# Kernel tuning notes

Hardware: AMD Instinct MI355X
Metric: run time of the kernel (lower is better)

Reference implementation:

```python
import jax, jax.numpy as jnp
import numpy as np


def setup_inputs() -> dict:
    key = jax.random.key(0)
    k1, k2, k3, k4 = jax.random.split(key, 4)
    B, T, C, H = 8, 2048, 1024, 128
    x = jax.random.normal(k1, (B, T, C), dtype=jnp.float32)
    Wq = jax.random.normal(k2, (C, H), dtype=jnp.float32) * (C ** -0.5)
    Wk = jax.random.normal(k3, (C, H), dtype=jnp.float32) * (C ** -0.5)
    Wv = jax.random.normal(k4, (C, H), dtype=jnp.float32) * (C ** -0.5)
    return {
        "x": x, "Wq": Wq, "Wk": Wk, "Wv": Wv,
        "gamma_fast_logit": jnp.float32(0.0),
        "gamma_medium_logit": jnp.float32(2.0),
        "gamma_slow_logit": jnp.float32(4.0),
        "alpha_logits": jnp.zeros((3,), dtype=jnp.float32),
    }


def _temporal_bias(T, gamma_fast_logit, gamma_medium_logit, gamma_slow_logit, alpha_logits):
    # delta_t[i,j] = max(i-j, 0)
    i = jnp.arange(T)[:, None]
    j = jnp.arange(T)[None, :]
    delta_t = jnp.maximum(i - j, 0).astype(jnp.float32)  # (T, T)
    gf = jax.nn.sigmoid(gamma_fast_logit) * 0.3 + 0.6
    gm = jax.nn.sigmoid(gamma_medium_logit) * 0.15 + 0.85
    gs = jax.nn.sigmoid(gamma_slow_logit) * 0.05 + 0.95
    alpha = jax.nn.softmax(alpha_logits)
    mix = (alpha[0] * jnp.power(gf, delta_t)
           + alpha[1] * jnp.power(gm, delta_t)
           + alpha[2] * jnp.power(gs, delta_t))
    return jnp.log(mix + 1e-8)  # (T, T)


def reference(x, Wq, Wk, Wv, gamma_fast_logit, gamma_medium_logit, gamma_slow_logit, alpha_logits):
    B, T, C = x.shape
    H = Wq.shape[1]
    q = x @ Wq  # (B, T, H)
    k = x @ Wk
    v = x @ Wv
    scale = H ** -0.5
    wei = jnp.einsum('bth,bsh->bts', q, k) * scale  # (B, T, T)
    bias = _temporal_bias(T, gamma_fast_logit, gamma_medium_logit, gamma_slow_logit, alpha_logits)
    wei = wei + bias[None, :, :]
    causal = jnp.tril(jnp.ones((T, T), dtype=bool))
    wei = jnp.where(causal[None, :, :], wei, -jnp.inf)
    wei = jax.nn.softmax(wei, axis=-1)
    out = jnp.einsum('bts,bsh->bth', wei, v)  # (B, T, H)
    return out
```

## Files before the change

### kernel.cpp

```cpp
#include <hip/hip_runtime.h>
#include <hip/hip_bf16.h>
#include <cstdint>

typedef __attribute__((ext_vector_type(8))) short bf16x8;
typedef __attribute__((ext_vector_type(4))) float f32x4;

#define T_SEQ 2048
#define NB    8
#define CDIM  1024
#define HDIM  128
#define NQB   32

__device__ __forceinline__ float exp2fast(float x) { return __builtin_amdgcn_exp2f(x); }
__device__ __forceinline__ float log2fast(float x) { return __builtin_amdgcn_logf(x); }

__device__ __forceinline__ short f2bf(float f) {
  unsigned u = __float_as_uint(f);
  u += 0x7fff + ((u >> 16) & 1);
  return (short)(u >> 16);
}

__device__ __forceinline__ float bf2f(short s) {
  return __uint_as_float(((unsigned)(unsigned short)s) << 16);
}

__device__ __forceinline__ unsigned pk2(float a, float b) {
  return (unsigned)(unsigned short)f2bf(a) | ((unsigned)(unsigned short)f2bf(b) << 16);
}

__device__ __forceinline__ void gload_lds16(const void* gsrc, void* lds_base_uniform) {
  __builtin_amdgcn_global_load_lds(
      (const __attribute__((address_space(1))) unsigned int*)gsrc,
      (__attribute__((address_space(3))) unsigned int*)lds_base_uniform,
      16, 0, 0);
}

__global__ void msta_bias_kernel(const float* gfl, const float* gml, const float* gsl,
                                 const float* al, float* tab) {
  int d = blockIdx.x * 256 + threadIdx.x;
  if (d >= T_SEQ) return;
  float gf = 0.30f / (1.f + __expf(-gfl[0])) + 0.60f;
  float gm = 0.15f / (1.f + __expf(-gml[0])) + 0.85f;
  float gs = 0.05f / (1.f + __expf(-gsl[0])) + 0.95f;
  float a0 = al[0], a1 = al[1], a2 = al[2];
  float mx = fmaxf(a0, fmaxf(a1, a2));
  float e0 = __expf(a0 - mx), e1 = __expf(a1 - mx), e2 = __expf(a2 - mx);
  float inv = 1.f / (e0 + e1 + e2);
  float fd = (float)d;
  float mix = e0 * inv * exp2fast(fd * log2fast(gf))
            + e1 * inv * exp2fast(fd * log2fast(gm))
            + e2 * inv * exp2fast(fd * log2fast(gs));
  tab[d] = log2fast(mix + 1e-8f);
}

__global__ void msta_wt_kernel(const float* Wq, const float* Wk, const float* Wv, short* wt) {
  int idx = blockIdx.x * 256 + threadIdx.x;
  int m = idx >> 17;
  int r = idx & 131071;
  int n = r >> 10;
  int kk = r & 1023;
  const float* W = (m == 0) ? Wq : ((m == 1) ? Wk : Wv);
  float v = W[kk * HDIM + n];
  if (m == 0) v *= 0.08838834764831845f * 1.4426950408889634f;
  wt[idx] = f2bf(v);
}

__global__ __launch_bounds__(256) void msta_qkv_kernel(
    const float* __restrict__ x, const short* __restrict__ wt,
    short* __restrict__ q, short* __restrict__ k, short* __restrict__ vt) {
  __shared__ short xs[2][64 * 64];
  __shared__ short wsm[2][128 * 64];

  const int tid  = threadIdx.x;
  const int lane = tid & 63;
  const int w    = tid >> 6;
  const int rh   = w >> 1, ch = w & 1;
  const int lo   = lane & 15, hi = lane >> 4;
  const int bid  = blockIdx.x;
  const int xcd  = bid & 7;
  const int j    = bid >> 3;
  const int m    = j % 3;
  const int r0   = (xcd * 32 + j / 3) * 64;

  const int xG0 = tid * 2;
  const int xr0_ = xG0 >> 3, xg0_ = xG0 & 7;
  const int xr1_ = (xG0 + 1) >> 3, xg1_ = (xG0 + 1) & 7;
  const float* xsrc0 = x + (size_t)(r0 + xr0_) * CDIM + xg0_ * 8;
  const float* xsrc1 = x + (size_t)(r0 + xr1_) * CDIM + xg1_ * 8;
  const int xd0 = xr0_ * 128 + ((xg0_ ^ (xr0_ & 7)) << 4);
  const int xd1 = xr1_ * 128 + ((xg1_ ^ (xr1_ & 7)) << 4);

  const char* wsrc[4];
  #pragma unroll
  for (int i = 0; i < 4; i++) {
    int G = (w * 4 + i) * 64 + lane;
    int n = G >> 3, g = G & 7;
    int c = g ^ (n & 7);
    wsrc[i] = (const char*)(wt + ((size_t)m * 128 + n) * CDIM) + c * 16;
  }

  f32x4 acc[2][4];
  #pragma unroll
  for (int f = 0; f < 2; f++)
    #pragma unroll
    for (int jf = 0; jf < 4; jf++)
      acc[f][jf] = (f32x4){0.f, 0.f, 0.f, 0.f};

  float4 xa0, xb0, xa1, xb1;
  auto xload = [&](int t) {
    const float* s0 = xsrc0 + t * 64;
    const float* s1 = xsrc1 + t * 64;
    xa0 = *(const float4*)s0; xb0 = *(const float4*)(s0 + 4);
    xa1 = *(const float4*)s1; xb1 = *(const float4*)(s1 + 4);
  };
  auto xwrite = [&](int buf) {
    uint4 u0, u1;
    u0.x = pk2(xa0.x, xa0.y); u0.y = pk2(xa0.z, xa0.w);
    u0.z = pk2(xb0.x, xb0.y); u0.w = pk2(xb0.z, xb0.w);
    u1.x = pk2(xa1.x, xa1.y); u1.y = pk2(xa1.z, xa1.w);
    u1.z = pk2(xb1.x, xb1.y); u1.w = pk2(xb1.z, xb1.w);
    *(uint4*)((char*)xs[buf] + xd0) = u0;
    *(uint4*)((char*)xs[buf] + xd1) = u1;
  };
  auto stageW = [&](int buf) {
    char* wd = (char*)wsm[buf];
    #pragma unroll
    for (int i = 0; i < 4; i++) {
      gload_lds16(wsrc[i], wd + (w * 4 + i) * 1024);
      wsrc[i] += 128;
    }
  };

  xload(0);
  stageW(0);
  xwrite(0);
  __syncthreads();

  #pragma unroll 2
  for (int t = 0; t < 16; ++t) {
    const int buf = t & 1;
    if (t < 15) { xload(t + 1); stageW(buf ^ 1); }

    #pragma unroll
    for (int kk = 0; kk < 2; kk++) {
      bf16x8 A[2];
      #pragma unroll
      for (int f = 0; f < 2; f++) {
        int r = rh * 32 + f * 16 + lo;
        A[f] = *(const bf16x8*)((const char*)xs[buf] + r * 128 +
                                ((kk * 64 + hi * 16) ^ ((r & 7) << 4)));
      }
      #pragma unroll
      for (int jf = 0; jf < 4; jf++) {
        int n = ch * 64 + jf * 16 + lo;
        int byteoff = n * 128 + ((kk * 64 + hi * 16) ^ ((n & 7) << 4));
        bf16x8 Bv = *(const bf16x8*)((const char*)wsm[buf] + byteoff);
        acc[0][jf] = __builtin_amdgcn_mfma_f32_16x16x32_bf16(A[0], Bv, acc[0][jf], 0, 0, 0);
        acc[1][jf] = __builtin_amdgcn_mfma_f32_16x16x32_bf16(A[1], Bv, acc[1][jf], 0, 0, 0);
      }
    }
    if (t < 15) xwrite(buf ^ 1);
    __syncthreads();
  }

  short* es = (short*)xs;
  if (m == 2) {
    #pragma unroll
    for (int f = 0; f < 2; f++) {
      #pragma unroll
      for (int jf = 0; jf < 4; jf++) {
        int col  = ch * 64 + jf * 16 + lo;
        int trow = rh * 32 + f * 16 + hi * 4;
        f32x4 a = acc[f][jf];
        uint2 pr;
        pr.x = pk2(a[0], a[1]);
        pr.y = pk2(a[2], a[3]);
        int byteoff = col * 128 + ((trow * 2) ^ ((col & 7) << 4));
        *(uint2*)((char*)es + byteoff) = pr;
      }
    }
    __syncthreads();
    const int bb = r0 >> 11, tt0 = r0 & 2047;
    short* vbase = vt + (size_t)bb * HDIM * T_SEQ + tt0;
    #pragma unroll
    for (int p = 0; p < 4; p++) {
      int col = (tid >> 3) + p * 32;
      int t8  = tid & 7;
      int byteoff = col * 128 + ((t8 * 16) ^ ((col & 7) << 4));
      *(bf16x8*)(vbase + (size_t)col * T_SEQ + t8 * 8) =
          *(const bf16x8*)((const char*)es + byteoff);
    }
  } else {
    short* dst = (m == 0) ? q : k;
    #pragma unroll
    for (int f = 0; f < 2; f++) {
      #pragma unroll
      for (int jf = 0; jf < 4; jf++) {
        int col   = ch * 64 + jf * 16 + lo;
        int trow0 = rh * 32 + f * 16 + hi * 4;
        f32x4 a = acc[f][jf];
        #pragma unroll
        for (int rg = 0; rg < 4; rg++)
          es[(trow0 + rg) * 128 + col] = f2bf(a[rg]);
      }
    }
    __syncthreads();
    #pragma unroll
    for (int p = 0; p < 4; p++) {
      int row = (tid >> 4) + p * 16;
      int c16 = tid & 15;
      *(bf16x8*)(dst + (size_t)(r0 + row) * HDIM + c16 * 8) =
          *(const bf16x8*)(es + row * 128 + c16 * 8);
    }
  }
}

template <int SP>
__global__ __launch_bounds__(256) void msta_attn_kernel(
    const short* __restrict__ q, const short* __restrict__ kg,
    const short* __restrict__ vt, const float* __restrict__ bias_tab,
    float* __restrict__ out, short* __restrict__ opart, float2* __restrict__ ml) {
  __shared__ short Ks[64 * 128];
  __shared__ short Vs[128 * 64];
  __shared__ short Ps[4][16 * 64];

  const int tid  = threadIdx.x;
  const int lane = tid & 63;
  const int w    = tid >> 6;
  const int lo   = lane & 15, hi = lane >> 4;

  const int idx = blockIdx.x;
  const int b   = idx & 7;
  const int r_  = idx >> 3;
  const int qb  = (NQB - 1) - r_ / SP;
  const int sp  = r_ % SP;
  const int q0  = qb * 64;

  const int nt  = qb + 1;
  const int csz = (nt + SP - 1) / SP;
  const int t0  = sp * csz;
  const int t1  = (t0 + csz < nt) ? (t0 + csz) : nt;

  if (t0 >= t1) {
    if (SP > 1 && lane < 16) {
      int t = q0 + w * 16 + lane;
      ml[((size_t)sp * NB + b) * T_SEQ + t] = make_float2(-1e30f, 0.f);
    }
    return;
  }

  const short* kb = kg + (size_t)b * T_SEQ * HDIM;
  const short* vb = vt + (size_t)b * HDIM * T_SEQ;

  bf16x8 qf[4];
  const short* qbase = q + ((size_t)b * T_SEQ + q0 + w * 16 + lo) * HDIM;
  #pragma unroll
  for (int ks = 0; ks < 4; ks++)
    qf[ks] = *(const bf16x8*)(qbase + ks * 32 + hi * 8);

  const int s0i = (t1 - 1) * 64;
  const char* ksrc[4];
  const char* vsrc[4];
  #pragma unroll
  for (int i = 0; i < 4; i++) {
    int G = (w * 4 + i) * 64 + lane;
    { int r = G >> 4, g = G & 15;
      int c = (g & 8) | ((g & 7) ^ (r & 7));
      ksrc[i] = (const char*)(kb + (size_t)(s0i + r) * HDIM) + c * 16; }
    { int r = G >> 3, g = G & 7;
      int c = g ^ (r & 7);
      vsrc[i] = (const char*)(vb + (size_t)r * T_SEQ + s0i) + c * 16; }
  }
  auto stage = [&]() {
    #pragma unroll
    for (int i = 0; i < 4; i++) {
      gload_lds16(ksrc[i], (char*)Ks + (w * 4 + i) * 1024);
      ksrc[i] -= 64 * HDIM * 2;
      gload_lds16(vsrc[i], (char*)Vs + (w * 4 + i) * 1024);
      vsrc[i] -= 128;
    }
  };

  f32x4 oacc[8];
  #pragma unroll
  for (int jo = 0; jo < 8; jo++) oacc[jo] = (f32x4){0.f, 0.f, 0.f, 0.f};
  float mrow[4], lrow[4];
  #pragma unroll
  for (int rg = 0; rg < 4; rg++) { mrow[rg] = -1e30f; lrow[rg] = 0.f; }

  stage();
  __syncthreads();

  for (int t = t1 - 1; t >= t0; --t) {
    const int s0 = t * 64;

    f32x4 sacc[4];
    #pragma unroll
    for (int jf = 0; jf < 4; jf++) sacc[jf] = (f32x4){0.f, 0.f, 0.f, 0.f};
    __builtin_amdgcn_s_setprio(1);
    #pragma unroll
    for (int ks = 0; ks < 4; ks++) {
      #pragma unroll
      for (int jf = 0; jf < 4; jf++) {
        int s = jf * 16 + lo;
        int byteoff = s * 256 + ((ks * 64 + hi * 16) ^ ((s & 7) << 4));
        bf16x8 kf = *(const bf16x8*)((const char*)Ks + byteoff);
        sacc[jf] = __builtin_amdgcn_mfma_f32_16x16x32_bf16(qf[ks], kf, sacc[jf], 0, 0, 0);
      }
    }
    __builtin_amdgcn_s_setprio(0);

    float sv[4][4];
    #pragma unroll
    for (int jf = 0; jf < 4; jf++) {
      #pragma unroll
      for (int rg = 0; rg < 4; rg++) {
        int i_ = q0 + w * 16 + hi * 4 + rg;
        int j_ = s0 + jf * 16 + lo;
        int d = i_ - j_;
        sv[jf][rg] = (d >= 0) ? (sacc[jf][rg] + bias_tab[d]) : -1e30f;
      }
    }

    float mx[4];
    bool need = false;
    #pragma unroll
    for (int rg = 0; rg < 4; rg++) {
      float v = fmaxf(fmaxf(sv[0][rg], sv[1][rg]), fmaxf(sv[2][rg], sv[3][rg]));
      v = fmaxf(v, __shfl_xor(v, 1));
      v = fmaxf(v, __shfl_xor(v, 2));
      v = fmaxf(v, __shfl_xor(v, 4));
      v = fmaxf(v, __shfl_xor(v, 8));
      mx[rg] = v;
      need |= (v > mrow[rg]);
    }
    if (__any((int)need)) {
      #pragma unroll
      for (int rg = 0; rg < 4; rg++) {
        float mnew = fmaxf(mrow[rg], mx[rg]);
        float sc = exp2fast(mrow[rg] - mnew);
        mrow[rg] = mnew;
        lrow[rg] *= sc;
        #pragma unroll
        for (int jo = 0; jo < 8; jo++) oacc[jo][rg] *= sc;
      }
    }

    float psum[4] = {0.f, 0.f, 0.f, 0.f};
    #pragma unroll
    for (int jf = 0; jf < 4; jf++) {
      #pragma unroll
      for (int rg = 0; rg < 4; rg++) {
        float p = exp2fast(sv[jf][rg] - mrow[rg]);
        psum[rg] += p;
        int prow = hi * 4 + rg;
        int pcol = jf * 16 + lo;
        int byteoff = prow * 128 + ((pcol * 2) ^ ((prow & 7) << 4));
        *(short*)((char*)Ps[w] + byteoff) = f2bf(p);
      }
    }
    #pragma unroll
    for (int rg = 0; rg < 4; rg++) {
      float s = psum[rg];
      s += __shfl_xor(s, 1); s += __shfl_xor(s, 2);
      s += __shfl_xor(s, 4); s += __shfl_xor(s, 8);
      lrow[rg] += s;
    }

    __builtin_amdgcn_s_setprio(1);
    #pragma unroll
    for (int ks = 0; ks < 2; ks++) {
      int pbyte = lo * 128 + ((ks * 64 + hi * 16) ^ ((lo & 7) << 4));
      bf16x8 pf = *(const bf16x8*)((const char*)Ps[w] + pbyte);
      #pragma unroll
      for (int jo = 0; jo < 8; jo++) {
        int h = jo * 16 + lo;
        int vbyte = h * 128 + ((ks * 64 + hi * 16) ^ ((h & 7) << 4));
        bf16x8 vf = *(const bf16x8*)((const char*)Vs + vbyte);
        oacc[jo] = __builtin_amdgcn_mfma_f32_16x16x32_bf16(pf, vf, oacc[jo], 0, 0, 0);
      }
    }
    __builtin_amdgcn_s_setprio(0);

    if (t > t0) {
      __syncthreads();
      stage();
      __syncthreads();
    }
  }

  if constexpr (SP == 1) {
    #pragma unroll
    for (int jo = 0; jo < 8; jo++) {
      #pragma unroll
      for (int rg = 0; rg < 4; rg++) {
        int t = q0 + w * 16 + hi * 4 + rg;
        out[((size_t)b * T_SEQ + t) * HDIM + jo * 16 + lo] = oacc[jo][rg] / lrow[rg];
      }
    }
  } else {
    #pragma unroll
    for (int jo = 0; jo < 8; jo++) {
      #pragma unroll
      for (int rg = 0; rg < 4; rg++) {
        int t = q0 + w * 16 + hi * 4 + rg;
        opart[(((size_t)sp * NB + b) * T_SEQ + t) * HDIM + jo * 16 + lo] = f2bf(oacc[jo][rg]);
      }
    }
    if (lo == 0) {
      #pragma unroll
      for (int rg = 0; rg < 4; rg++) {
        int t = q0 + w * 16 + hi * 4 + rg;
        ml[((size_t)sp * NB + b) * T_SEQ + t] = make_float2(mrow[rg], lrow[rg]);
      }
    }
  }
}

template <int SP>
__global__ __launch_bounds__(256) void msta_merge_kernel(
    const short* __restrict__ opart, const float2* __restrict__ ml,
    float* __restrict__ out) {
  int id  = blockIdx.x * 256 + threadIdx.x;
  int row = id >> 5;
  int c4  = id & 31;

  float2 v[SP];
  float m = -1e30f;
  #pragma unroll
  for (int sp = 0; sp < SP; sp++) {
    v[sp] = ml[(size_t)sp * (NB * T_SEQ) + row];
    if (v[sp].y > 0.f) m = fmaxf(m, v[sp].x);
  }
  float denom = 0.f;
  float wgt[SP];
  #pragma unroll
  for (int sp = 0; sp < SP; sp++) {
    wgt[sp] = (v[sp].y > 0.f) ? exp2fast(v[sp].x - m) : 0.f;
    denom += wgt[sp] * v[sp].y;
  }
  float4 acc = {0.f, 0.f, 0.f, 0.f};
  #pragma unroll
  for (int sp = 0; sp < SP; sp++) {
    if (wgt[sp] != 0.f) {
      ushort4 o = *(const ushort4*)(opart + ((size_t)sp * (NB * T_SEQ) + row) * HDIM + c4 * 4);
      acc.x += wgt[sp] * bf2f((short)o.x); acc.y += wgt[sp] * bf2f((short)o.y);
      acc.z += wgt[sp] * bf2f((short)o.z); acc.w += wgt[sp] * bf2f((short)o.w);
    }
  }
  float inv = 1.f / denom;
  float4 r = make_float4(acc.x * inv, acc.y * inv, acc.z * inv, acc.w * inv);
  *(float4*)(out + (size_t)row * HDIM + c4 * 4) = r;
}

extern "C" void kernel_launch(void* const* d_in, const int* in_sizes, int n_in,
                              void* d_out, int out_size, void* d_ws, size_t ws_size,
                              hipStream_t stream) {
  (void)in_sizes; (void)n_in; (void)out_size;
  const float* x   = (const float*)d_in[0];
  const float* Wq  = (const float*)d_in[1];
  const float* Wk  = (const float*)d_in[2];
  const float* Wv  = (const float*)d_in[3];
  const float* gfl = (const float*)d_in[4];
  const float* gml = (const float*)d_in[5];
  const float* gsl = (const float*)d_in[6];
  const float* al  = (const float*)d_in[7];
  float* out = (float*)d_out;

  char* wsb = (char*)d_ws;
  float*  bias_tab = (float*)wsb;
  short*  qw   = (short*)(wsb + 8192);
  short*  kw   = (short*)(wsb + 8192 + 1 * 4194304);
  short*  vtw  = (short*)(wsb + 8192 + 2 * 4194304);
  short*  wtw  = (short*)(wsb + 8192 + 3 * 4194304);
  short*  opart = (short*)(wsb + 13639680);

  const size_t need8 = 13639680 + 8ull * 4194304 + 8ull * 131072;
  const size_t need4 = 13639680 + 4ull * 4194304 + 4ull * 131072;

  msta_bias_kernel<<<8, 256, 0, stream>>>(gfl, gml, gsl, al, bias_tab);
  msta_wt_kernel<<<1536, 256, 0, stream>>>(Wq, Wk, Wv, wtw);
  msta_qkv_kernel<<<768, 256, 0, stream>>>(x, wtw, qw, kw, vtw);

  if (ws_size >= need8) {
    float2* mlp = (float2*)(wsb + 13639680 + 8ull * 4194304);
    msta_attn_kernel<8><<<NB * NQB * 8, 256, 0, stream>>>(qw, kw, vtw, bias_tab,
                                                          nullptr, opart, mlp);
    msta_merge_kernel<8><<<(NB * T_SEQ * 32) / 256, 256, 0, stream>>>(opart, mlp, out);
  } else if (ws_size >= need4) {
    float2* mlp = (float2*)(wsb + 13639680 + 4ull * 4194304);
    msta_attn_kernel<4><<<NB * NQB * 4, 256, 0, stream>>>(qw, kw, vtw, bias_tab,
                                                          nullptr, opart, mlp);
    msta_merge_kernel<4><<<(NB * T_SEQ * 32) / 256, 256, 0, stream>>>(opart, mlp, out);
  } else {
    msta_attn_kernel<1><<<NB * NQB, 256, 0, stream>>>(qw, kw, vtw, bias_tab,
                                                      out, nullptr, nullptr);
  }
}
```

Measured before the change: 85.47 us.

## Stage fp32 x tiles directly to LDS and drop double buffering in QKV projection

The QKV projection kernel now copies raw fp32 x tiles into shared memory with direct global-to-LDS loads, using a 16-way XOR swizzle. The bf16 conversion moves to the point where MFMA operands are read. Both the x and W staging lose their double buffering: each K-step loads, synchronises, computes and synchronises again. This drops the register round-trip and pack/store path for x, but global loads no longer overlap with compute, and each A fragment is now converted again on every read.

```diff
diff --git a/kernel.cpp b/kernel.cpp
--- a/kernel.cpp
+++ b/kernel.cpp
@@ -68,8 +68,8 @@
 __global__ __launch_bounds__(256) void msta_qkv_kernel(
     const float* __restrict__ x, const short* __restrict__ wt,
     short* __restrict__ q, short* __restrict__ k, short* __restrict__ vt) {
-  __shared__ short xs[2][64 * 64];
-  __shared__ short wsm[2][128 * 64];
+  __shared__ float xs[64 * 64];
+  __shared__ short wsm[128 * 64];
 
   const int tid  = threadIdx.x;
   const int lane = tid & 63;
@@ -82,21 +82,17 @@
   const int m    = j % 3;
   const int r0   = (xcd * 32 + j / 3) * 64;
 
-  const int xG0 = tid * 2;
-  const int xr0_ = xG0 >> 3, xg0_ = xG0 & 7;
-  const int xr1_ = (xG0 + 1) >> 3, xg1_ = (xG0 + 1) & 7;
-  const float* xsrc0 = x + (size_t)(r0 + xr0_) * CDIM + xg0_ * 8;
-  const float* xsrc1 = x + (size_t)(r0 + xr1_) * CDIM + xg1_ * 8;
-  const int xd0 = xr0_ * 128 + ((xg0_ ^ (xr0_ & 7)) << 4);
-  const int xd1 = xr1_ * 128 + ((xg1_ ^ (xr1_ & 7)) << 4);
-
+  const char* xsrc[4];
   const char* wsrc[4];
   #pragma unroll
   for (int i = 0; i < 4; i++) {
     int G = (w * 4 + i) * 64 + lane;
-    int n = G >> 3, g = G & 7;
-    int c = g ^ (n & 7);
-    wsrc[i] = (const char*)(wt + ((size_t)m * 128 + n) * CDIM) + c * 16;
+    { int r = G >> 4, g = G & 15;
+      int c = g ^ (r & 15);
+      xsrc[i] = (const char*)(x + (size_t)(r0 + r) * CDIM) + c * 16; }
+    { int n = G >> 3, g = G & 7;
+      int c = g ^ (n & 7);
+      wsrc[i] = (const char*)(wt + ((size_t)m * 128 + n) * CDIM) + c * 16; }
   }
 
   f32x4 acc[2][4];
@@ -106,40 +102,15 @@
     for (int jf = 0; jf < 4; jf++)
       acc[f][jf] = (f32x4){0.f, 0.f, 0.f, 0.f};
 
-  float4 xa0, xb0, xa1, xb1;
-  auto xload = [&](int t) {
-    const float* s0 = xsrc0 + t * 64;
-    const float* s1 = xsrc1 + t * 64;
-    xa0 = *(const float4*)s0; xb0 = *(const float4*)(s0 + 4);
-    xa1 = *(const float4*)s1; xb1 = *(const float4*)(s1 + 4);
-  };
-  auto xwrite = [&](int buf) {
-    uint4 u0, u1;
-    u0.x = pk2(xa0.x, xa0.y); u0.y = pk2(xa0.z, xa0.w);
-    u0.z = pk2(xb0.x, xb0.y); u0.w = pk2(xb0.z, xb0.w);
-    u1.x = pk2(xa1.x, xa1.y); u1.y = pk2(xa1.z, xa1.w);
-    u1.z = pk2(xb1.x, xb1.y); u1.w = pk2(xb1.z, xb1.w);
-    *(uint4*)((char*)xs[buf] + xd0) = u0;
-    *(uint4*)((char*)xs[buf] + xd1) = u1;
-  };
-  auto stageW = [&](int buf) {
-    char* wd = (char*)wsm[buf];
+  for (int t = 0; t < 16; ++t) {
     #pragma unroll
     for (int i = 0; i < 4; i++) {
-      gload_lds16(wsrc[i], wd + (w * 4 + i) * 1024);
+      gload_lds16(xsrc[i], (char*)xs + (w * 4 + i) * 1024);
+      xsrc[i] += 256;
+      gload_lds16(wsrc[i], (char*)wsm + (w * 4 + i) * 1024);
       wsrc[i] += 128;
     }
-  };
-
-  xload(0);
-  stageW(0);
-  xwrite(0);
-  __syncthreads();
-
-  #pragma unroll 2
-  for (int t = 0; t < 16; ++t) {
-    const int buf = t & 1;
-    if (t < 15) { xload(t + 1); stageW(buf ^ 1); }
+    __syncthreads();
 
     #pragma unroll
     for (int kk = 0; kk < 2; kk++) {
@@ -147,19 +118,25 @@
       #pragma unroll
       for (int f = 0; f < 2; f++) {
         int r = rh * 32 + f * 16 + lo;
-        A[f] = *(const bf16x8*)((const char*)xs[buf] + r * 128 +
-                                ((kk * 64 + hi * 16) ^ ((r & 7) << 4)));
+        int g0 = kk * 8 + hi * 2;
+        int sw = r & 15;
+        const char* base = (const char*)xs + r * 256;
+        float4 a0 = *(const float4*)(base + (((g0)     ^ sw) << 4));
+        float4 a1 = *(const float4*)(base + (((g0 + 1) ^ sw) << 4));
+        uint4 u;
+        u.x = pk2(a0.x, a0.y); u.y = pk2(a0.z, a0.w);
+        u.z = pk2(a1.x, a1.y); u.w = pk2(a1.z, a1.w);
+        A[f] = *(bf16x8*)&u;
       }
       #pragma unroll
       for (int jf = 0; jf < 4; jf++) {
         int n = ch * 64 + jf * 16 + lo;
         int byteoff = n * 128 + ((kk * 64 + hi * 16) ^ ((n & 7) << 4));
-        bf16x8 Bv = *(const bf16x8*)((const char*)wsm[buf] + byteoff);
+        bf16x8 Bv = *(const bf16x8*)((const char*)wsm + byteoff);
         acc[0][jf] = __builtin_amdgcn_mfma_f32_16x16x32_bf16(A[0], Bv, acc[0][jf], 0, 0, 0);
         acc[1][jf] = __builtin_amdgcn_mfma_f32_16x16x32_bf16(A[1], Bv, acc[1][jf], 0, 0, 0);
       }
     }
-    if (t < 15) xwrite(buf ^ 1);
     __syncthreads();
   }
 
```

After: 84.60 us. No clear change (-1.0%).
